# Kernel optimization log

Measured on AMD Instinct MI355X. Metric: run time of the kernel, lower is better.

## Reference

```python
import jax, jax.numpy as jnp
import numpy as np

N = 50000      # nodes
E = 800000     # edges (before self-loops)
IN_DIM = 256
HID = 128
HEADS = 4
HEAD_D = HID // HEADS
LAYERS = 2
EPS = 1e-5
SLOPE = 0.2    # GATv2 leaky_relu negative slope (PyG default)


def setup_inputs() -> dict:
    key = jax.random.key(0)
    ks = jax.random.split(key, 8)
    x = jax.random.normal(ks[0], (N, IN_DIM), dtype=jnp.float32)
    edge_index = jax.random.randint(ks[1], (2, E), 0, N, dtype=jnp.int64)
    s_in = (2.0 / (IN_DIM + HID)) ** 0.5
    s_h = (2.0 / (HID + HID)) ** 0.5
    return {
        'x': x,
        'W_in': jax.random.normal(ks[2], (IN_DIM, HID), dtype=jnp.float32) * s_in,
        'b_in': jnp.zeros((HID,), jnp.float32),
        'ln_in_g': jnp.ones((HID,), jnp.float32),
        'ln_in_b': jnp.zeros((HID,), jnp.float32),
        'Wl': jax.random.normal(ks[3], (LAYERS, HID, HID), dtype=jnp.float32) * s_h,
        'Wr': jax.random.normal(ks[4], (LAYERS, HID, HID), dtype=jnp.float32) * s_h,
        'att': jax.random.normal(ks[5], (LAYERS, HEADS, HEAD_D), dtype=jnp.float32) * s_h,
        'ln_g': jnp.ones((LAYERS, HID), jnp.float32),
        'ln_b': jnp.zeros((LAYERS, HID), jnp.float32),
        'edge_index': edge_index,
    }


def layer_norm(h, g, b):
    mu = jnp.mean(h, axis=-1, keepdims=True)
    var = jnp.mean(jnp.square(h - mu), axis=-1, keepdims=True)
    return (h - mu) * jax.lax.rsqrt(var + EPS) * g + b


def gatv2_conv(h, src, dst, Wl, Wr, att):
    # h: [N, HID]; src/dst: [E'] (self-loops included)
    xl = (h @ Wl).reshape(N, HEADS, HEAD_D)   # source transform (also message)
    xr = (h @ Wr).reshape(N, HEADS, HEAD_D)   # target transform
    e = jax.nn.leaky_relu(xl[src] + xr[dst], SLOPE)          # [E', H, D]
    logits = jnp.einsum('ehd,hd->eh', e, att)                # [E', H]
    # segment softmax over incoming edges of each dst node
    m = jax.lax.stop_gradient(jax.ops.segment_max(logits, dst, num_segments=N))
    a = jnp.exp(logits - m[dst])
    z = jax.ops.segment_sum(a, dst, num_segments=N)
    alpha = a / z[dst]                                       # [E', H]
    out = jax.ops.segment_sum(xl[src] * alpha[:, :, None], dst, num_segments=N)
    return out.reshape(N, HID)


def reference(x, W_in, b_in, ln_in_g, ln_in_b, Wl, Wr, att, ln_g, ln_b, edge_index):
    loops = jnp.arange(N, dtype=edge_index.dtype)
    src = jnp.concatenate([edge_index[0], loops])
    dst = jnp.concatenate([edge_index[1], loops])
    h = jax.nn.relu(layer_norm(x @ W_in + b_in, ln_in_g, ln_in_b))
    for l in range(LAYERS):
        h_new = jax.nn.elu(layer_norm(gatv2_conv(h, src, dst, Wl[l], Wr[l], att[l]), ln_g[l], ln_b[l]))
        h = h + h_new
    return h
```

## Files before the change

### kernel.cpp

```cpp
#include <hip/hip_runtime.h>
#include <hip/hip_bf16.h>


#define NN 50000
#define EE 800000
#define EP (EE + NN)
#define IN_DIM 256
#define HID 128
#define SLOPE 0.2f
#define LN_EPS 1e-5f
#define NB 196
#define L2E 1.4426950408889634f

typedef short s8v __attribute__((ext_vector_type(8)));
typedef float f4v __attribute__((ext_vector_type(4)));

__device__ __forceinline__ float u2f(unsigned int u) {
    union { unsigned int i; float f; } c; c.i = u; return c.f;
}
__device__ __forceinline__ unsigned short f2bf(float f) {
    union { float f; unsigned int i; } c; c.f = f;
    unsigned int r = (c.i + 0x7fffu + ((c.i >> 16) & 1u)) >> 16;
    return (unsigned short)r;
}
__device__ __forceinline__ void unpack8(const uint4 raw, float* m) {
    m[0] = u2f(raw.x << 16); m[1] = u2f(raw.x & 0xffff0000u);
    m[2] = u2f(raw.y << 16); m[3] = u2f(raw.y & 0xffff0000u);
    m[4] = u2f(raw.z << 16); m[5] = u2f(raw.z & 0xffff0000u);
    m[6] = u2f(raw.w << 16); m[7] = u2f(raw.w & 0xffff0000u);
}

__global__ void prep_weights(const float* __restrict__ Win,
                             const float* __restrict__ Wl,
                             const float* __restrict__ Wr,
                             float4* __restrict__ wp) {
    const int sid = blockIdx.x * 256 + threadIdx.x;
    const float* W;
    int slot;
    if (sid < 4096) { W = Win; slot = sid; }
    else {
        const int m = (sid - 4096) >> 11;
        slot = (sid - 4096) & 2047;
        W = (m == 0) ? Wl : (m == 1) ? Wr : (m == 2) ? (Wl + 16384) : (Wr + 16384);
    }
    const int n = slot & 127;
    const int kbase = (slot >> 9) * 32 + ((slot >> 7) & 3) * 8;
    unsigned short o[8];
#pragma unroll
    for (int j = 0; j < 8; j++) o[j] = f2bf(W[(size_t)(kbase + j) * 128 + n]);
    wp[sid] = *(const float4*)o;
}

__global__ __launch_bounds__(256) void gemm_in_mfma(
        const float* __restrict__ x,
        const float4* __restrict__ wp,
        const float* __restrict__ bin,
        const float* __restrict__ g,
        const float* __restrict__ bb,
        unsigned short* __restrict__ hb) {
    __shared__ s8v wlds[4096];
    const int tid = threadIdx.x;
    const int wv = tid >> 6, lane = tid & 63;
    const int l15 = lane & 15, kseg = lane >> 4;
    const int row0 = blockIdx.x * 64 + wv * 16;
    const int arow = row0 + l15;
    const int r = (arow < NN) ? arow : 0;

    s8v afrag[8];
#pragma unroll
    for (int ks = 0; ks < 8; ks++) {
        const float* ap = x + (size_t)r * IN_DIM + ks * 32 + kseg * 8;
        const float4 a0 = *(const float4*)ap;
        const float4 a1 = *(const float4*)(ap + 4);
        unsigned short t[8] = { f2bf(a0.x), f2bf(a0.y), f2bf(a0.z), f2bf(a0.w),
                                f2bf(a1.x), f2bf(a1.y), f2bf(a1.z), f2bf(a1.w) };
        afrag[ks] = *(const s8v*)t;
    }

#pragma unroll
    for (int i = 0; i < 16; i++) {
        const int idx = i * 256 + tid;
        ((float4*)wlds)[idx] = wp[idx];
    }
    __syncthreads();

    f4v acc[8];
#pragma unroll
    for (int nb = 0; nb < 8; nb++) acc[nb] = (f4v){0.f, 0.f, 0.f, 0.f};
#pragma unroll
    for (int ks = 0; ks < 8; ks++) {
#pragma unroll
        for (int nb = 0; nb < 8; nb++) {
            const s8v bfrag = wlds[(ks * 4 + kseg) * 128 + nb * 16 + l15];
            acc[nb] = __builtin_amdgcn_mfma_f32_16x16x32_bf16(afrag[ks], bfrag, acc[nb], 0, 0, 0);
        }
    }

    float binv[8], gv[8], bbv[8];
#pragma unroll
    for (int nb = 0; nb < 8; nb++) {
        const int col = nb * 16 + l15;
        binv[nb] = bin[col]; gv[nb] = g[col]; bbv[nb] = bb[col];
    }
    float s1[4] = {0.f, 0.f, 0.f, 0.f}, s2[4] = {0.f, 0.f, 0.f, 0.f};
#pragma unroll
    for (int nb = 0; nb < 8; nb++)
#pragma unroll
        for (int reg = 0; reg < 4; reg++) {
            const float t = acc[nb][reg] + binv[nb];
            acc[nb][reg] = t;
            s1[reg] += t; s2[reg] += t * t;
        }
#pragma unroll
    for (int off = 1; off < 16; off <<= 1)
#pragma unroll
        for (int reg = 0; reg < 4; reg++) {
            s1[reg] += __shfl_xor(s1[reg], off);
            s2[reg] += __shfl_xor(s2[reg], off);
        }
    float mu[4], rstd[4];
#pragma unroll
    for (int reg = 0; reg < 4; reg++) {
        mu[reg] = s1[reg] / (float)HID;
        rstd[reg] = rsqrtf(s2[reg] / (float)HID - mu[reg] * mu[reg] + LN_EPS);
    }
    const int rbase = row0 + 4 * kseg;
#pragma unroll
    for (int reg = 0; reg < 4; reg++) {
        const int grow = rbase + reg;
        if (grow >= NN) continue;
#pragma unroll
        for (int nb = 0; nb < 8; nb++) {
            const int col = nb * 16 + l15;
            float v = (acc[nb][reg] - mu[reg]) * rstd[reg] * gv[nb] + bbv[nb];
            hb[(size_t)grow * HID + col] = f2bf(fmaxf(v, 0.f));
        }
    }
}

__global__ __launch_bounds__(256) void gemm_xlxr_mfma(
        const unsigned short* __restrict__ hb,
        const float4* __restrict__ wp,
        unsigned short* __restrict__ xl,
        unsigned short* __restrict__ xrb) {
    __shared__ s8v wlds[4096];
    const int tid = threadIdx.x;
    const int wv = tid >> 6, lane = tid & 63;
    const int l15 = lane & 15, kseg = lane >> 4;
    const int row0 = blockIdx.x * 64 + wv * 16;
    const int arow = row0 + l15;
    const int r = (arow < NN) ? arow : 0;

    s8v afrag[4];
#pragma unroll
    for (int ks = 0; ks < 4; ks++)
        afrag[ks] = *(const s8v*)(hb + (size_t)r * HID + ks * 32 + kseg * 8);

#pragma unroll
    for (int i = 0; i < 16; i++) {
        const int idx = i * 256 + tid;
        ((float4*)wlds)[idx] = wp[idx];
    }
    __syncthreads();

    f4v accL[8], accR[8];
#pragma unroll
    for (int nb = 0; nb < 8; nb++) {
        accL[nb] = (f4v){0.f, 0.f, 0.f, 0.f};
        accR[nb] = (f4v){0.f, 0.f, 0.f, 0.f};
    }
#pragma unroll
    for (int ks = 0; ks < 4; ks++) {
#pragma unroll
        for (int nb = 0; nb < 8; nb++) {
            const s8v bL = wlds[(ks * 4 + kseg) * 128 + nb * 16 + l15];
            accL[nb] = __builtin_amdgcn_mfma_f32_16x16x32_bf16(afrag[ks], bL, accL[nb], 0, 0, 0);
            const s8v bR = wlds[2048 + (ks * 4 + kseg) * 128 + nb * 16 + l15];
            accR[nb] = __builtin_amdgcn_mfma_f32_16x16x32_bf16(afrag[ks], bR, accR[nb], 0, 0, 0);
        }
    }

    const int rbase = row0 + 4 * kseg;
#pragma unroll
    for (int reg = 0; reg < 4; reg++) {
        const int grow = rbase + reg;
        if (grow >= NN) continue;
#pragma unroll
        for (int nb = 0; nb < 8; nb++) {
            const int col = nb * 16 + l15;
            xl[(size_t)grow * HID + col]  = f2bf(accL[nb][reg]);
            xrb[(size_t)grow * HID + col] = f2bf(accR[nb][reg]);
        }
    }
}

__global__ void dst_hist(const int* __restrict__ ei, int* __restrict__ cnt) {
    const long e = (long)blockIdx.x * 256 + threadIdx.x;
    if (e >= EP) return;
    const int d = (e < EE) ? ei[EE + e] : (int)(e - EE);
    atomicAdd(&cnt[d], 1);
}

__global__ void scan_bsum(const int* __restrict__ cnt, int* __restrict__ bsum) {
    const int tid = threadIdx.x;
    const int i = blockIdx.x * 256 + tid;
    int v = (i < NN) ? cnt[i] : 0;
#pragma unroll
    for (int off = 1; off < 64; off <<= 1) v += __shfl_xor(v, off);
    __shared__ int ws[4];
    if ((tid & 63) == 0) ws[tid >> 6] = v;
    __syncthreads();
    if (tid == 0) bsum[blockIdx.x] = ws[0] + ws[1] + ws[2] + ws[3];
}

__global__ void scan_bpre(const int* __restrict__ bsum, int* __restrict__ bpre) {
    const int t = threadIdx.x;
    const int lane = t & 63, wv = t >> 6;
    const int v = (t < NB) ? bsum[t] : 0;
    int s = v;
#pragma unroll
    for (int off = 1; off < 64; off <<= 1) {
        const int u = __shfl_up(s, off);
        if (lane >= off) s += u;
    }
    __shared__ int wt[4];
    if (lane == 63) wt[wv] = s;
    __syncthreads();
    int add = 0;
    for (int w = 0; w < wv; w++) add += wt[w];
    if (t < NB) bpre[t] = s + add - v;
}

__global__ void scan_rowptr(const int* __restrict__ cnt,
                            const int* __restrict__ bpre,
                            int* __restrict__ rowptr) {
    const int tid = threadIdx.x;
    const int lane = tid & 63, wv = tid >> 6;
    const int i = blockIdx.x * 256 + tid;
    const int v = (i < NN) ? cnt[i] : 0;
    int s = v;
#pragma unroll
    for (int off = 1; off < 64; off <<= 1) {
        const int u = __shfl_up(s, off);
        if (lane >= off) s += u;
    }
    __shared__ int wt[4];
    if (lane == 63) wt[wv] = s;
    __syncthreads();
    int add = bpre[blockIdx.x];
    for (int w = 0; w < wv; w++) add += wt[w];
    const int excl = s + add - v;
    if (i < NN) rowptr[i] = excl;
    if (i == NN - 1) rowptr[NN] = excl + v;
}

__global__ void csr_scatter(const int* __restrict__ ei,
                            const int* __restrict__ rowptr,
                            int* __restrict__ fill,
                            int* __restrict__ esrcb) {
    const long e = (long)blockIdx.x * 256 + threadIdx.x;
    if (e >= EP) return;
    int s, d;
    if (e < EE) { s = ei[e]; d = ei[EE + e]; }
    else        { s = d = (int)(e - EE); }
    const int pos = atomicAdd(&fill[d], 1);
    esrcb[rowptr[d] + pos] = s * (HID * 2);
}

__global__ __launch_bounds__(256) void gat_ln(
        const unsigned short* __restrict__ xl,
        const unsigned short* __restrict__ xrb,
        const float* __restrict__ att,
        const int* __restrict__ rowptr,
        const int* __restrict__ esrcb,
        const float* __restrict__ g,
        const float* __restrict__ b,
        const unsigned short* __restrict__ hres,
        float* __restrict__ dest,
        unsigned short* __restrict__ destb) {
    const int tid = threadIdx.x;
    const int lane = tid & 63;
    const int wv = tid >> 6;
    const int l16 = lane & 15;
    const int grp = lane >> 4;
    const int node = blockIdx.x * 16 + wv * 4 + grp;
    const int f0 = l16 * 8;

    float xrv[8], a06[8], a04[8];
    {
        const uint4 xraw = *(const uint4*)(xrb + (size_t)node * HID + f0);
        unpack8(xraw, xrv);
        const float4 t0 = *(const float4*)(att + f0);
        const float4 t1 = *(const float4*)(att + f0 + 4);
        float av[8] = { t0.x, t0.y, t0.z, t0.w, t1.x, t1.y, t1.z, t1.w };
#pragma unroll
        for (int j = 0; j < 8; j++) {
            a06[j] = 0.6f * L2E * av[j];
            a04[j] = 0.4f * L2E * av[j];
        }
    }
    const int beg = rowptr[node];
    const int deg = rowptr[node + 1] - beg;
    int dmax = deg;
    dmax = max(dmax, __shfl_xor(dmax, 16));
    dmax = max(dmax, __shfl_xor(dmax, 32));

    const char* xlbase = (const char*)xl + f0 * 2;
    const int gb = lane & 48;

    float acc[8];
#pragma unroll
    for (int j = 0; j < 8; j++) acc[j] = 0.f;
    float z = 0.f;

    int sb = (l16 < deg) ? esrcb[beg + l16] : 0;

#define PROCR(RAW, VALID) do {                                              \
        float m[8];                                                         \
        unpack8((RAW), m);                                                  \
        float v = 0.f;                                                      \
        _Pragma("unroll")                                                   \
        for (int j = 0; j < 8; j++) {                                       \
            const float tt = m[j] + xrv[j];                                 \
            v += tt * a06[j] + fabsf(tt) * a04[j];                          \
        }                                                                   \
        v += __shfl_xor(v, 1);                                              \
        v += __shfl_xor(v, 2);                          \
        const float a = (VALID) ? __builtin_amdgcn_exp2f(v) : 0.f;          \
        z += a;                                                             \
        _Pragma("unroll")                                                   \
        for (int j = 0; j < 8; j++) acc[j] = fmaf(a, m[j], acc[j]);         \
    } while (0)

    for (int t = 0; t < dmax; t += 4) {
        if ((t & 15) == 0 && t) {
            sb = (t + l16 < deg) ? esrcb[beg + t + l16] : 0;
        }
        const int o0 = __shfl(sb, gb | ((t + 0) & 15));
        const int o1 = __shfl(sb, gb | ((t + 1) & 15));
        const int o2 = __shfl(sb, gb | ((t + 2) & 15));
        const int o3 = __shfl(sb, gb | ((t + 3) & 15));
        const uint4 r0 = *(const uint4*)(xlbase + o0);
        const uint4 r1 = *(const uint4*)(xlbase + o1);
        const uint4 r2 = *(const uint4*)(xlbase + o2);
        const uint4 r3 = *(const uint4*)(xlbase + o3);
        PROCR(r0, t + 0 < deg);
        PROCR(r1, t + 1 < deg);
        PROCR(r2, t + 2 < deg);
        PROCR(r3, t + 3 < deg);
    }
#undef PROCR

    const float inv = 1.f / z;
    float o[8];
    float s1 = 0.f, s2 = 0.f;
#pragma unroll
    for (int j = 0; j < 8; j++) {
        o[j] = acc[j] * inv;
        s1 += o[j];
        s2 = fmaf(o[j], o[j], s2);
    }
#pragma unroll
    for (int off = 1; off < 16; off <<= 1) {
        s1 += __shfl_xor(s1, off);
        s2 += __shfl_xor(s2, off);
    }
    const float mu = s1 / (float)HID;
    const float rstd = rsqrtf(s2 / (float)HID - mu * mu + LN_EPS);

    float gv[8], bv[8], hv[8];
    {
        const float4 g0 = *(const float4*)(g + f0);
        const float4 g1 = *(const float4*)(g + f0 + 4);
        gv[0]=g0.x; gv[1]=g0.y; gv[2]=g0.z; gv[3]=g0.w;
        gv[4]=g1.x; gv[5]=g1.y; gv[6]=g1.z; gv[7]=g1.w;
        const float4 b0 = *(const float4*)(b + f0);
        const float4 b1 = *(const float4*)(b + f0 + 4);
        bv[0]=b0.x; bv[1]=b0.y; bv[2]=b0.z; bv[3]=b0.w;
        bv[4]=b1.x; bv[5]=b1.y; bv[6]=b1.z; bv[7]=b1.w;
        const uint4 hraw = *(const uint4*)(hres + (size_t)node * HID + f0);
        unpack8(hraw, hv);
    }
    float res[8];
#pragma unroll
    for (int j = 0; j < 8; j++) {
        float n = (o[j] - mu) * rstd * gv[j] + bv[j];
        n = (n > 0.f) ? n : (__builtin_amdgcn_exp2f(n * L2E) - 1.f);
        res[j] = hv[j] + n;
    }
    if (dest) {
        float* dp = dest + (size_t)node * HID + f0;
        *(float4*)dp       = (float4){res[0], res[1], res[2], res[3]};
        *(float4*)(dp + 4) = (float4){res[4], res[5], res[6], res[7]};
    }
    if (destb) {
        unsigned short o16[8];
#pragma unroll
        for (int j = 0; j < 8; j++) o16[j] = f2bf(res[j]);
        *(uint4*)(destb + (size_t)node * HID + f0) = *(const uint4*)o16;
    }
}

extern "C" void kernel_launch(void* const* d_in, const int* in_sizes, int n_in,
                              void* d_out, int out_size, void* d_ws, size_t ws_size,
                              hipStream_t stream) {
    const float* x       = (const float*)d_in[0];
    const float* W_in    = (const float*)d_in[1];
    const float* b_in    = (const float*)d_in[2];
    const float* ln_in_g = (const float*)d_in[3];
    const float* ln_in_b = (const float*)d_in[4];
    const float* Wl      = (const float*)d_in[5];
    const float* Wr      = (const float*)d_in[6];
    const float* att     = (const float*)d_in[7];
    const float* ln_g    = (const float*)d_in[8];
    const float* ln_b    = (const float*)d_in[9];
    const int*   ei      = (const int*)d_in[10];
    float* out = (float*)d_out;

    unsigned short* hb  = (unsigned short*)d_ws;
    unsigned short* hb2 = hb  + (size_t)NN * HID;
    unsigned short* xlb = hb2 + (size_t)NN * HID;
    unsigned short* xrb = xlb + (size_t)NN * HID;
    float4* wp = (float4*)(xrb + (size_t)NN * HID);
    int* cnt    = (int*)(wp + 12288);
    int* fill   = cnt + NN;
    int* rowptr = fill + NN;
    int* bsum   = rowptr + (NN + 1);
    int* bpre   = bsum + NB;
    int* esrcb  = bpre + NB;

    prep_weights<<<48, 256, 0, stream>>>(W_in, Wl, Wr, wp);

    (void)hipMemsetAsync(cnt, 0, 2 * NN * sizeof(int), stream);
    const int eblocks = (EP + 255) / 256;
    dst_hist<<<eblocks, 256, 0, stream>>>(ei, cnt);
    scan_bsum<<<NB, 256, 0, stream>>>(cnt, bsum);
    scan_bpre<<<1, 256, 0, stream>>>(bsum, bpre);
    scan_rowptr<<<NB, 256, 0, stream>>>(cnt, bpre, rowptr);
    csr_scatter<<<eblocks, 256, 0, stream>>>(ei, rowptr, fill, esrcb);

    const int mblocks = (NN + 63) / 64;
    gemm_in_mfma<<<mblocks, 256, 0, stream>>>(x, wp, b_in, ln_in_g, ln_in_b, hb);

    for (int l = 0; l < 2; l++) {
        const unsigned short* hsrc = (l == 0) ? hb : hb2;
        gemm_xlxr_mfma<<<mblocks, 256, 0, stream>>>(hsrc, wp + 4096 + l * 4096, xlb, xrb);
        gat_ln<<<NN / 16, 256, 0, stream>>>(xlb, xrb, att + (size_t)l * HID,
                                            rowptr, esrcb,
                                            ln_g + (size_t)l * HID,
                                            ln_b + (size_t)l * HID,
                                            hsrc,
                                            (l == 1) ? out : (float*)nullptr,
                                            (l == 0) ? hb2 : (unsigned short*)nullptr);
    }
}
```

Before: 219.3 us.

## Degree-sort nodes for GAT load balance and compact CSR to 16-bit sources

Three preprocessing kernels (degree histogram, scan, scatter) build a permutation of nodes sorted by in-degree. gat_ln then handles nodes in that order, so the four nodes sharing a wavefront have similar degrees and less of the loop runs idle up to the slowest node. The histogram kernel now records each edge's slot within its node, which removes the second atomic in the CSR scatter. Source indices are stored as 16-bit values and shifted into byte offsets in the kernel, halving index traffic. In exchange there are extra small launches, and per-node reads of xr, residual and output become scattered rather than sequential.

```diff
diff --git a/kernel.cpp b/kernel.cpp
--- a/kernel.cpp
+++ b/kernel.cpp
@@ -10,6 +10,7 @@
 #define SLOPE 0.2f
 #define LN_EPS 1e-5f
 #define NB 196
+#define DB 1024
 #define L2E 1.4426950408889634f
 
 typedef short s8v __attribute__((ext_vector_type(8)));
@@ -194,11 +195,12 @@
     }
 }
 
-__global__ void dst_hist(const int* __restrict__ ei, int* __restrict__ cnt) {
+__global__ void dst_hist(const int* __restrict__ ei, int* __restrict__ cnt,
+                         unsigned short* __restrict__ epos) {
     const long e = (long)blockIdx.x * 256 + threadIdx.x;
     if (e >= EP) return;
     const int d = (e < EE) ? ei[EE + e] : (int)(e - EE);
-    atomicAdd(&cnt[d], 1);
+    epos[e] = (unsigned short)atomicAdd(&cnt[d], 1);
 }
 
 __global__ void scan_bsum(const int* __restrict__ cnt, int* __restrict__ bsum) {
@@ -256,15 +258,49 @@
 
 __global__ void csr_scatter(const int* __restrict__ ei,
                             const int* __restrict__ rowptr,
-                            int* __restrict__ fill,
-                            int* __restrict__ esrcb) {
+                            const unsigned short* __restrict__ epos,
+                            unsigned short* __restrict__ esrc16) {
     const long e = (long)blockIdx.x * 256 + threadIdx.x;
     if (e >= EP) return;
     int s, d;
     if (e < EE) { s = ei[e]; d = ei[EE + e]; }
     else        { s = d = (int)(e - EE); }
-    const int pos = atomicAdd(&fill[d], 1);
-    esrcb[rowptr[d] + pos] = s * (HID * 2);
+    esrc16[rowptr[d] + epos[e]] = (unsigned short)s;
+}
+
+__global__ void deg_hist(const int* __restrict__ cnt, int* __restrict__ dhist) {
+    const int i = blockIdx.x * 256 + threadIdx.x;
+    if (i >= NN) return;
+    atomicAdd(&dhist[min(cnt[i], DB - 1)], 1);
+}
+
+__global__ void deg_scan(const int* __restrict__ dhist, int* __restrict__ dbase) {
+    const int t = threadIdx.x;
+    const int lane = t & 63, w = t >> 6;
+    const int v = dhist[t];
+    int s = v;
+#pragma unroll
+    for (int off = 1; off < 64; off <<= 1) {
+        const int u = __shfl_up(s, off);
+        if (lane >= off) s += u;
+    }
+    __shared__ int wt[16];
+    if (lane == 63) wt[w] = s;
+    __syncthreads();
+    int add = 0;
+    for (int k = 0; k < w; k++) add += wt[k];
+    dbase[t] = s + add - v;
+}
+
+__global__ void perm_scatter(const int* __restrict__ cnt,
+                             const int* __restrict__ dbase,
+                             int* __restrict__ dfill,
+                             int* __restrict__ perm) {
+    const int i = blockIdx.x * 256 + threadIdx.x;
+    if (i >= NN) return;
+    const int d = min(cnt[i], DB - 1);
+    const int pos = atomicAdd(&dfill[d], 1);
+    perm[dbase[d] + pos] = i;
 }
 
 __global__ __launch_bounds__(256) void gat_ln(
@@ -272,7 +308,8 @@
         const unsigned short* __restrict__ xrb,
         const float* __restrict__ att,
         const int* __restrict__ rowptr,
-        const int* __restrict__ esrcb,
+        const unsigned short* __restrict__ esrc16,
+        const int* __restrict__ perm,
         const float* __restrict__ g,
         const float* __restrict__ b,
         const unsigned short* __restrict__ hres,
@@ -283,7 +320,7 @@
     const int wv = tid >> 6;
     const int l16 = lane & 15;
     const int grp = lane >> 4;
-    const int node = blockIdx.x * 16 + wv * 4 + grp;
+    const int node = perm[blockIdx.x * 16 + wv * 4 + grp];
     const int f0 = l16 * 8;
 
     float xrv[8], a06[8], a04[8];
@@ -313,7 +350,7 @@
     for (int j = 0; j < 8; j++) acc[j] = 0.f;
     float z = 0.f;
 
-    int sb = (l16 < deg) ? esrcb[beg + l16] : 0;
+    int sb = (l16 < deg) ? (int)esrc16[beg + l16] : 0;
 
 #define PROCR(RAW, VALID) do {                                              \
         float m[8];                                                         \
@@ -334,12 +371,12 @@
 
     for (int t = 0; t < dmax; t += 4) {
         if ((t & 15) == 0 && t) {
-            sb = (t + l16 < deg) ? esrcb[beg + t + l16] : 0;
-        }
-        const int o0 = __shfl(sb, gb | ((t + 0) & 15));
-        const int o1 = __shfl(sb, gb | ((t + 1) & 15));
-        const int o2 = __shfl(sb, gb | ((t + 2) & 15));
-        const int o3 = __shfl(sb, gb | ((t + 3) & 15));
+            sb = (t + l16 < deg) ? (int)esrc16[beg + t + l16] : 0;
+        }
+        const int o0 = __shfl(sb, gb | ((t + 0) & 15)) << 8;
+        const int o1 = __shfl(sb, gb | ((t + 1) & 15)) << 8;
+        const int o2 = __shfl(sb, gb | ((t + 2) & 15)) << 8;
+        const int o3 = __shfl(sb, gb | ((t + 3) & 15)) << 8;
         const uint4 r0 = *(const uint4*)(xlbase + o0);
         const uint4 r1 = *(const uint4*)(xlbase + o1);
         const uint4 r2 = *(const uint4*)(xlbase + o2);
@@ -423,21 +460,29 @@
     unsigned short* xrb = xlb + (size_t)NN * HID;
     float4* wp = (float4*)(xrb + (size_t)NN * HID);
     int* cnt    = (int*)(wp + 12288);
-    int* fill   = cnt + NN;
-    int* rowptr = fill + NN;
+    int* dhist  = cnt + NN;
+    int* dfill  = dhist + DB;
+    int* rowptr = dfill + DB;
     int* bsum   = rowptr + (NN + 1);
     int* bpre   = bsum + NB;
-    int* esrcb  = bpre + NB;
+    int* dbase  = bpre + NB;
+    int* perm   = dbase + DB;
+    unsigned short* epos   = (unsigned short*)(perm + NN);
+    unsigned short* esrc16 = epos + EP;
 
     prep_weights<<<48, 256, 0, stream>>>(W_in, Wl, Wr, wp);
 
-    (void)hipMemsetAsync(cnt, 0, 2 * NN * sizeof(int), stream);
+    (void)hipMemsetAsync(cnt, 0, (NN + 2 * DB) * sizeof(int), stream);
     const int eblocks = (EP + 255) / 256;
-    dst_hist<<<eblocks, 256, 0, stream>>>(ei, cnt);
+    dst_hist<<<eblocks, 256, 0, stream>>>(ei, cnt, epos);
     scan_bsum<<<NB, 256, 0, stream>>>(cnt, bsum);
     scan_bpre<<<1, 256, 0, stream>>>(bsum, bpre);
     scan_rowptr<<<NB, 256, 0, stream>>>(cnt, bpre, rowptr);
-    csr_scatter<<<eblocks, 256, 0, stream>>>(ei, rowptr, fill, esrcb);
+    csr_scatter<<<eblocks, 256, 0, stream>>>(ei, rowptr, epos, esrc16);
+
+    deg_hist<<<NB, 256, 0, stream>>>(cnt, dhist);
+    deg_scan<<<1, DB, 0, stream>>>(dhist, dbase);
+    perm_scatter<<<NB, 256, 0, stream>>>(cnt, dbase, dfill, perm);
 
     const int mblocks = (NN + 63) / 64;
     gemm_in_mfma<<<mblocks, 256, 0, stream>>>(x, wp, b_in, ln_in_g, ln_in_b, hb);
@@ -446,7 +491,7 @@
         const unsigned short* hsrc = (l == 0) ? hb : hb2;
         gemm_xlxr_mfma<<<mblocks, 256, 0, stream>>>(hsrc, wp + 4096 + l * 4096, xlb, xrb);
         gat_ln<<<NN / 16, 256, 0, stream>>>(xlb, xrb, att + (size_t)l * HID,
-                                            rowptr, esrcb,
+                                            rowptr, esrc16, perm,
                                             ln_g + (size_t)l * HID,
                                             ln_b + (size_t)l * HID,
                                             hsrc,
```

Result: slower. 430.8 us (+96.5%).
